# Performance work log

Hardware: AMD Instinct MI355X
Metric: run time of the kernel (lower is better)

Reference implementation:

```python
import jax, jax.numpy as jnp
import numpy as np

N_NODES = 20000
N_EDGES = 320000
IN_DIM = 512
HID = 256
N_GRAPHS = 256


def setup_inputs() -> dict:
    key = jax.random.key(0)
    ks = jax.random.split(key, 7)
    x = jax.random.normal(ks[0], (N_NODES, IN_DIM), dtype=jnp.float32)
    edge_index = jax.random.randint(ks[1], (2, N_EDGES), 0, N_NODES, dtype=jnp.int64)
    batch = jnp.sort(jax.random.randint(ks[2], (N_NODES,), 0, N_GRAPHS, dtype=jnp.int64))
    W = jax.random.normal(ks[3], (IN_DIM, HID), dtype=jnp.float32) * (1.0 / np.sqrt(IN_DIM))
    b = jax.random.normal(ks[4], (HID,), dtype=jnp.float32) * 0.02
    lin_w = jax.random.normal(ks[5], (HID, 1), dtype=jnp.float32) * (1.0 / np.sqrt(HID))
    lin_b = jax.random.normal(ks[6], (1,), dtype=jnp.float32) * 0.02
    return {"x": x, "edge_index": edge_index, "batch": batch,
            "W": W, "b": b, "lin_w": lin_w, "lin_b": lin_b}


def reference(x, edge_index, batch, W, b, lin_w, lin_b):
    N = x.shape[0]
    # --- GCNConv: add self-loops, symmetric normalization ---
    loop = jnp.arange(N, dtype=edge_index.dtype)
    src = jnp.concatenate([edge_index[0], loop])   # [E+N]
    dst = jnp.concatenate([edge_index[1], loop])   # [E+N]
    deg = jax.ops.segment_sum(jnp.ones_like(dst, dtype=x.dtype), dst, num_segments=N)
    dinv = jnp.where(deg > 0, jax.lax.rsqrt(deg), 0.0)          # [N]
    norm = dinv[src] * dinv[dst]                                 # [E+N]
    h = x @ W                                                    # [N, HID] dense GEMM
    msgs = h[src] * norm[:, None]                                # gather + scale
    agg = jax.ops.segment_sum(msgs, dst, num_segments=N) + b     # scatter-add
    xr = jax.nn.relu(agg)                                        # [N, HID]
    # --- global_mean_pool over graph ids ---
    sums = jax.ops.segment_sum(xr, batch, num_segments=N_GRAPHS)             # [G, HID]
    counts = jax.ops.segment_sum(jnp.ones((N,), dtype=x.dtype), batch, num_segments=N_GRAPHS)
    pooled = sums / jnp.maximum(counts, 1.0)[:, None]
    # --- linear head + sigmoid ---
    out = jax.nn.sigmoid(pooled @ lin_w + lin_b)                 # [G, 1]
    return out.reshape(-1)
```

## Files before the change

kernel.cpp:

```cpp
#include <hip/hip_runtime.h>
#include <hip/hip_bf16.h>
#include <cstdint>

typedef __attribute__((ext_vector_type(8))) _Float16 half8;
typedef __attribute__((ext_vector_type(2))) float f32x2;
typedef __attribute__((ext_vector_type(4))) float f32x4;

#define N_NODES 20000
#define N_EDGES 320000
#define IN_DIM 512
#define HID 256
#define N_GRAPHS 256
#define NPB 8
#define ECH 1024
#define BSTR 40

#define PREP_W   (IN_DIM * HID)
#define PREP_E   (PREP_W + N_EDGES)
#define PREP_B   (PREP_E + N_NODES)
__global__ __launch_bounds__(256) void prep_kernel(const float* __restrict__ W,
                                                   const int* __restrict__ dst,
                                                   const int* __restrict__ batch,
                                                   _Float16* __restrict__ wt,
                                                   int* __restrict__ ecnt,
                                                   int* __restrict__ counts) {
    int t = blockIdx.x * 256 + threadIdx.x;
    if (t < PREP_W) {
        wt[t] = (_Float16)W[(t & 511) * HID + (t >> 9)];
    } else if (t < PREP_E) {
        atomicAdd(&ecnt[dst[t - PREP_W]], 1);
    } else if (t < PREP_B) {
        atomicAdd(&counts[batch[t - PREP_E]], 1);
    }
}

__global__ __launch_bounds__(1024) void scan_dinv_kernel(const int* __restrict__ ecnt,
                                                         int* __restrict__ offsets,
                                                         float* __restrict__ dinv) {
    __shared__ int wsum[16];
    int t = threadIdx.x;
    int lane = t & 63, wid = t >> 6;
    const int CHS = 20;
    int base = t * CHS;
    int vals[CHS];
    int s = 0;
    if (t < 1000) {
        const int4* p = reinterpret_cast<const int4*>(ecnt + base);
#pragma unroll
        for (int i = 0; i < 5; ++i) {
            int4 v = p[i];
            vals[4*i+0] = v.x; vals[4*i+1] = v.y; vals[4*i+2] = v.z; vals[4*i+3] = v.w;
        }
#pragma unroll
        for (int i = 0; i < CHS; ++i) s += vals[i];
    }
    int incl = s;
#pragma unroll
    for (int off = 1; off < 64; off <<= 1) {
        int u = __shfl_up(incl, off, 64);
        if (lane >= off) incl += u;
    }
    if (lane == 63) wsum[wid] = incl;
    __syncthreads();
    if (t < 16) {
        int v = wsum[t];
#pragma unroll
        for (int off = 1; off < 16; off <<= 1) {
            int u = __shfl_up(v, off, 16);
            if (t >= off) v += u;
        }
        wsum[t] = v;
    }
    __syncthreads();
    int woff = (wid == 0) ? 0 : wsum[wid - 1];
    if (t < 1000) {
        int run = woff + incl - s;
#pragma unroll
        for (int i = 0; i < CHS; ++i) {
            int idx = base + i;
            offsets[idx] = run;
            dinv[idx] = rsqrtf((float)(vals[i] + 1));
            run += vals[i];
        }
    }
    if (t == 1023) offsets[N_NODES] = wsum[15];
}

#define GEMM_BLOCKS ((N_NODES + 63) / 64)
#define CSR_BLOCKS  ((N_EDGES + 255) / 256)
__global__ __launch_bounds__(256) void gemm_csr_kernel(const float* __restrict__ x,
                                                       const _Float16* __restrict__ wt,
                                                       unsigned char* __restrict__ h8,
                                                       const int* __restrict__ src,
                                                       const int* __restrict__ dst,
                                                       const float* __restrict__ dinv,
                                                       const int* __restrict__ offsets,
                                                       int* __restrict__ cnt2,
                                                       int2* __restrict__ csr) {
    __shared__ _Float16 bsl[256 * BSTR];
    if (blockIdx.x >= GEMM_BLOCKS) {
        int e = (blockIdx.x - GEMM_BLOCKS) * 256 + threadIdx.x;
        if (e < N_EDGES) {
            int s = src[e], d = dst[e];
            int slot = offsets[d] + atomicAdd(&cnt2[d], 1);
            int2 pk;
            pk.x = s;
            pk.y = __float_as_int(dinv[s] * dinv[d]);
            csr[slot] = pk;
        }
        return;
    }
    const int K = IN_DIM;
    int t    = threadIdx.x;
    int wave = t >> 6;
    int lane = t & 63;
    int col  = lane & 15;
    int quad = lane >> 4;
    int row0 = blockIdx.x * 64 + wave * 16;

    f32x4 acc[16];
#pragma unroll
    for (int i = 0; i < 16; ++i) acc[i] = (f32x4){0.f, 0.f, 0.f, 0.f};

    int arow = row0 + col;
    if (arow >= N_NODES) arow = N_NODES - 1;
    const float* aptr = x + (size_t)arow * K + quad * 8;
    const uint4* wsrc = reinterpret_cast<const uint4*>(wt + (size_t)t * K);

    float4 pa0 = *reinterpret_cast<const float4*>(aptr);
    float4 pa1 = *reinterpret_cast<const float4*>(aptr + 4);
    uint4 b0 = wsrc[0], b1 = wsrc[1], b2 = wsrc[2], b3 = wsrc[3];

    for (int k0 = 0; k0 < K; k0 += 32) {
        __syncthreads();
        {
            uint4* d = reinterpret_cast<uint4*>(&bsl[t * BSTR]);
            d[0] = b0; d[1] = b1; d[2] = b2; d[3] = b3;
        }
        __syncthreads();
        half8 xf;
        xf[0] = (_Float16)pa0.x; xf[1] = (_Float16)pa0.y;
        xf[2] = (_Float16)pa0.z; xf[3] = (_Float16)pa0.w;
        xf[4] = (_Float16)pa1.x; xf[5] = (_Float16)pa1.y;
        xf[6] = (_Float16)pa1.z; xf[7] = (_Float16)pa1.w;
        if (k0 + 32 < K) {
            const float* ap = aptr + k0 + 32;
            pa0 = *reinterpret_cast<const float4*>(ap);
            pa1 = *reinterpret_cast<const float4*>(ap + 4);
            const uint4* ws = wsrc + ((k0 + 32) >> 3);
            b0 = ws[0]; b1 = ws[1]; b2 = ws[2]; b3 = ws[3];
        }
#pragma unroll
        for (int nt = 0; nt < 16; ++nt) {
            half8 wf = *reinterpret_cast<const half8*>(
                &bsl[(nt * 16 + col) * BSTR + quad * 8]);
            acc[nt] = __builtin_amdgcn_mfma_f32_16x16x32_f16(wf, xf, acc[nt], 0, 0, 0);
        }
    }

    int node = row0 + col;
    if (node < N_NODES) {
        int fb = quad * 4;
        unsigned char* hrow = h8 + (size_t)node * HID + fb;
#pragma unroll
        for (int nt = 0; nt < 16; ++nt) {
            int u = __builtin_amdgcn_cvt_pk_fp8_f32(acc[nt][0], acc[nt][1], 0, false);
            u = __builtin_amdgcn_cvt_pk_fp8_f32(acc[nt][2], acc[nt][3], u, true);
            *reinterpret_cast<unsigned int*>(hrow + nt * 16) = (unsigned int)u;
        }
    }
}

__global__ __launch_bounds__(256, 8) void aggregate_kernel(const unsigned char* __restrict__ h8,
                                                           const float* __restrict__ bias,
                                                           const float* __restrict__ dinv,
                                                           const int* __restrict__ offsets,
                                                           const int2* __restrict__ csr,
                                                           const int* __restrict__ batch,
                                                           float* __restrict__ sums) {
    __shared__ int2 s_e[ECH];
    float* pool = reinterpret_cast<float*>(s_e);
    int v0  = blockIdx.x * NPB;
    int t   = threadIdx.x;
    int grp = t >> 6;
    int fl  = t & 63;
    int vg  = v0 + grp * 2;
    const float4 bf = *reinterpret_cast<const float4*>(bias + 4 * fl);

    int off[3];
#pragma unroll
    for (int i = 0; i <= 2; ++i) off[i] = offsets[vg + i];
    int beg0 = offsets[v0], end0 = offsets[v0 + NPB];

    float a0[2], a1[2], a2[2], a3[2];
#pragma unroll
    for (int i = 0; i < 2; ++i) {
        int v = vg + i;
        float dv = dinv[v];
        float d2 = dv * dv;
        unsigned int u = *reinterpret_cast<const unsigned int*>(h8 + (size_t)v * HID + 4 * fl);
        f32x2 lo = __builtin_amdgcn_cvt_pk_f32_fp8(u, false);
        f32x2 hi = __builtin_amdgcn_cvt_pk_f32_fp8(u, true);
        a0[i] = d2 * lo[0]; a1[i] = d2 * lo[1];
        a2[i] = d2 * hi[0]; a3[i] = d2 * hi[1];
    }

    for (int cb = beg0; cb < end0; cb += ECH) {
        int n = min(ECH, end0 - cb);
        for (int tt = t; tt < n; tt += 256) s_e[tt] = csr[cb + tt];
        __syncthreads();
#pragma unroll
        for (int i = 0; i < 2; ++i) {
            int lo_ = off[i] - cb;     if (lo_ < 0) lo_ = 0;
            int hi_ = off[i + 1] - cb; if (hi_ > n) hi_ = n;
            float x0 = a0[i], x1 = a1[i], x2 = a2[i], x3 = a3[i];
            int j = lo_;
            for (; j + 8 <= hi_; j += 8) {
#pragma unroll
                for (int q = 0; q < 8; ++q) {
                    int2 e = s_e[j + q];
                    unsigned int u = *reinterpret_cast<const unsigned int*>(
                        h8 + (size_t)e.x * HID + 4 * fl);
                    float w = __int_as_float(e.y);
                    f32x2 lo = __builtin_amdgcn_cvt_pk_f32_fp8(u, false);
                    f32x2 hi = __builtin_amdgcn_cvt_pk_f32_fp8(u, true);
                    x0 += w * lo[0]; x1 += w * lo[1];
                    x2 += w * hi[0]; x3 += w * hi[1];
                }
            }
            for (; j < hi_; ++j) {
                int2 e = s_e[j];
                unsigned int u = *reinterpret_cast<const unsigned int*>(
                    h8 + (size_t)e.x * HID + 4 * fl);
                float w = __int_as_float(e.y);
                f32x2 lo = __builtin_amdgcn_cvt_pk_f32_fp8(u, false);
                f32x2 hi = __builtin_amdgcn_cvt_pk_f32_fp8(u, true);
                x0 += w * lo[0]; x1 += w * lo[1];
                x2 += w * hi[0]; x3 += w * hi[1];
            }
            a0[i] = x0; a1[i] = x1; a2[i] = x2; a3[i] = x3;
        }
        __syncthreads();
    }

#pragma unroll
    for (int i = 0; i < 2; ++i) {
        f32x4 r;
        r[0] = fmaxf(a0[i] + bf.x, 0.f);
        r[1] = fmaxf(a1[i] + bf.y, 0.f);
        r[2] = fmaxf(a2[i] + bf.z, 0.f);
        r[3] = fmaxf(a3[i] + bf.w, 0.f);
        *reinterpret_cast<f32x4*>(&pool[(grp * 2 + i) * HID + 4 * fl]) = r;
    }
    __syncthreads();

    float acc = 0.f;
    int cur_g = batch[v0];
#pragma unroll
    for (int i = 0; i < NPB; ++i) {
        float val = pool[i * HID + t];
        int g = batch[v0 + i];
        if (g != cur_g) {
            atomicAdd(&sums[(size_t)cur_g * HID + t], acc);
            acc = 0.f;
            cur_g = g;
        }
        acc += val;
    }
    atomicAdd(&sums[(size_t)cur_g * HID + t], acc);
}

__global__ __launch_bounds__(256) void head_kernel(const float* __restrict__ sums,
                                                   const int* __restrict__ counts,
                                                   const float* __restrict__ lin_w,
                                                   const float* __restrict__ lin_b,
                                                   float* __restrict__ out) {
    int g = blockIdx.x;
    int f = threadIdx.x;
    float c = (float)counts[g];
    if (c < 1.f) c = 1.f;
    float v = (sums[(size_t)g * HID + f] / c) * lin_w[f];
#pragma unroll
    for (int off = 32; off >= 1; off >>= 1) v += __shfl_down(v, off, 64);
    __shared__ float red[4];
    if ((f & 63) == 0) red[f >> 6] = v;
    __syncthreads();
    if (f == 0) {
        float s = red[0] + red[1] + red[2] + red[3] + lin_b[0];
        out[g] = 1.0f / (1.0f + expf(-s));
    }
}

extern "C" void kernel_launch(void* const* d_in, const int* in_sizes, int n_in,
                              void* d_out, int out_size, void* d_ws, size_t ws_size,
                              hipStream_t stream) {
    const float* x     = (const float*)d_in[0];
    const int*   edge  = (const int*)d_in[1];
    const int*   batch = (const int*)d_in[2];
    const float* W     = (const float*)d_in[3];
    const float* b     = (const float*)d_in[4];
    const float* lin_w = (const float*)d_in[5];
    const float* lin_b = (const float*)d_in[6];
    float*       out   = (float*)d_out;

    const int N = N_NODES, E = N_EDGES, G = N_GRAPHS, K = IN_DIM, H = HID;
    const int* src = edge;
    const int* dst = edge + E;

    char* p = (char*)d_ws;
    auto alloc = [&](size_t bytes) {
        char* r = p;
        p += (bytes + 255) & ~(size_t)255;
        return r;
    };
    _Float16*      wt      = (_Float16*)alloc((size_t)H * K * 2);
    unsigned char* h8      = (unsigned char*)alloc((size_t)N * H);
    float*         dinv    = (float*)alloc((size_t)N * 4);
    int*           offsets = (int*)alloc((size_t)(N + 1) * 4);
    int2*          csr     = (int2*)alloc((size_t)E * 8);
    char* z0 = p;
    int*   ecnt   = (int*)alloc((size_t)N * 4);
    int*   cnt2   = (int*)alloc((size_t)N * 4);
    float* sums   = (float*)alloc((size_t)G * H * 4);
    int*   counts = (int*)alloc((size_t)G * 4);
    size_t zbytes = (size_t)(p - z0);

    hipMemsetAsync(z0, 0, zbytes, stream);

    prep_kernel<<<(PREP_B + 255) / 256, 256, 0, stream>>>(W, dst, batch, wt, ecnt, counts);
    scan_dinv_kernel<<<1, 1024, 0, stream>>>(ecnt, offsets, dinv);
    gemm_csr_kernel<<<GEMM_BLOCKS + CSR_BLOCKS, 256, 0, stream>>>(x, wt, h8, src, dst,
                                                                  dinv, offsets, cnt2, csr);
    aggregate_kernel<<<N / NPB, 256, 0, stream>>>(h8, b, dinv, offsets, csr, batch, sums);
    head_kernel<<<G, 256, 0, stream>>>(sums, counts, lin_w, lin_b, out);
}
```

Measured before the change: 186.2 us.

## Split GEMM and CSR fill into separate kernels with 16-row GEMM tiles

Separates the fused GEMM/CSR-fill launch into two kernels. The GEMM tile shrinks from 64 rows to 16 rows per block, with each wave covering a quarter of the output columns, so there are four times as many blocks and only 4 accumulators per thread. The W transpose in prep now reads coalesced and writes scattered. The aim is better occupancy and load balance for the GEMM, at the cost of loading the full W tile into shared memory for every 16 rows and paying one extra launch.

```diff
diff --git a/kernel.cpp b/kernel.cpp
--- a/kernel.cpp
+++ b/kernel.cpp
@@ -26,7 +26,8 @@
                                                    int* __restrict__ counts) {
     int t = blockIdx.x * 256 + threadIdx.x;
     if (t < PREP_W) {
-        wt[t] = (_Float16)W[(t & 511) * HID + (t >> 9)];
+        int k = t >> 8, n = t & 255;
+        wt[n * IN_DIM + k] = (_Float16)W[t];
     } else if (t < PREP_E) {
         atomicAdd(&ecnt[dst[t - PREP_W]], 1);
     } else if (t < PREP_B) {
@@ -86,44 +87,41 @@
     if (t == 1023) offsets[N_NODES] = wsum[15];
 }
 
-#define GEMM_BLOCKS ((N_NODES + 63) / 64)
-#define CSR_BLOCKS  ((N_EDGES + 255) / 256)
-__global__ __launch_bounds__(256) void gemm_csr_kernel(const float* __restrict__ x,
-                                                       const _Float16* __restrict__ wt,
-                                                       unsigned char* __restrict__ h8,
-                                                       const int* __restrict__ src,
+__global__ __launch_bounds__(256) void csr_fill_kernel(const int* __restrict__ src,
                                                        const int* __restrict__ dst,
                                                        const float* __restrict__ dinv,
                                                        const int* __restrict__ offsets,
                                                        int* __restrict__ cnt2,
                                                        int2* __restrict__ csr) {
+    int e = blockIdx.x * 256 + threadIdx.x;
+    if (e < N_EDGES) {
+        int s = src[e], d = dst[e];
+        int slot = offsets[d] + atomicAdd(&cnt2[d], 1);
+        int2 pk;
+        pk.x = s;
+        pk.y = __float_as_int(dinv[s] * dinv[d]);
+        csr[slot] = pk;
+    }
+}
+
+#define GEMM_BLOCKS (N_NODES / 16)
+__global__ __launch_bounds__(256) void gemm_kernel(const float* __restrict__ x,
+                                                   const _Float16* __restrict__ wt,
+                                                   unsigned char* __restrict__ h8) {
     __shared__ _Float16 bsl[256 * BSTR];
-    if (blockIdx.x >= GEMM_BLOCKS) {
-        int e = (blockIdx.x - GEMM_BLOCKS) * 256 + threadIdx.x;
-        if (e < N_EDGES) {
-            int s = src[e], d = dst[e];
-            int slot = offsets[d] + atomicAdd(&cnt2[d], 1);
-            int2 pk;
-            pk.x = s;
-            pk.y = __float_as_int(dinv[s] * dinv[d]);
-            csr[slot] = pk;
-        }
-        return;
-    }
     const int K = IN_DIM;
     int t    = threadIdx.x;
     int wave = t >> 6;
     int lane = t & 63;
     int col  = lane & 15;
     int quad = lane >> 4;
-    int row0 = blockIdx.x * 64 + wave * 16;
-
-    f32x4 acc[16];
-#pragma unroll
-    for (int i = 0; i < 16; ++i) acc[i] = (f32x4){0.f, 0.f, 0.f, 0.f};
+    int row0 = blockIdx.x * 16;
+
+    f32x4 acc[4];
+#pragma unroll
+    for (int i = 0; i < 4; ++i) acc[i] = (f32x4){0.f, 0.f, 0.f, 0.f};
 
     int arow = row0 + col;
-    if (arow >= N_NODES) arow = N_NODES - 1;
     const float* aptr = x + (size_t)arow * K + quad * 8;
     const uint4* wsrc = reinterpret_cast<const uint4*>(wt + (size_t)t * K);
 
@@ -151,23 +149,21 @@
             b0 = ws[0]; b1 = ws[1]; b2 = ws[2]; b3 = ws[3];
         }
 #pragma unroll
-        for (int nt = 0; nt < 16; ++nt) {
+        for (int i = 0; i < 4; ++i) {
+            int nt = wave * 4 + i;
             half8 wf = *reinterpret_cast<const half8*>(
                 &bsl[(nt * 16 + col) * BSTR + quad * 8]);
-            acc[nt] = __builtin_amdgcn_mfma_f32_16x16x32_f16(wf, xf, acc[nt], 0, 0, 0);
+            acc[i] = __builtin_amdgcn_mfma_f32_16x16x32_f16(wf, xf, acc[i], 0, 0, 0);
         }
     }
 
     int node = row0 + col;
-    if (node < N_NODES) {
-        int fb = quad * 4;
-        unsigned char* hrow = h8 + (size_t)node * HID + fb;
-#pragma unroll
-        for (int nt = 0; nt < 16; ++nt) {
-            int u = __builtin_amdgcn_cvt_pk_fp8_f32(acc[nt][0], acc[nt][1], 0, false);
-            u = __builtin_amdgcn_cvt_pk_fp8_f32(acc[nt][2], acc[nt][3], u, true);
-            *reinterpret_cast<unsigned int*>(hrow + nt * 16) = (unsigned int)u;
-        }
+    unsigned char* hrow = h8 + (size_t)node * HID + wave * 64 + quad * 4;
+#pragma unroll
+    for (int i = 0; i < 4; ++i) {
+        int u = __builtin_amdgcn_cvt_pk_fp8_f32(acc[i][0], acc[i][1], 0, false);
+        u = __builtin_amdgcn_cvt_pk_fp8_f32(acc[i][2], acc[i][3], u, true);
+        *reinterpret_cast<unsigned int*>(hrow + i * 16) = (unsigned int)u;
     }
 }
 
@@ -329,8 +325,8 @@
 
     prep_kernel<<<(PREP_B + 255) / 256, 256, 0, stream>>>(W, dst, batch, wt, ecnt, counts);
     scan_dinv_kernel<<<1, 1024, 0, stream>>>(ecnt, offsets, dinv);
-    gemm_csr_kernel<<<GEMM_BLOCKS + CSR_BLOCKS, 256, 0, stream>>>(x, wt, h8, src, dst,
-                                                                  dinv, offsets, cnt2, csr);
+    csr_fill_kernel<<<(E + 255) / 256, 256, 0, stream>>>(src, dst, dinv, offsets, cnt2, csr);
+    gemm_kernel<<<GEMM_BLOCKS, 256, 0, stream>>>(x, wt, h8);
     aggregate_kernel<<<N / NPB, 256, 0, stream>>>(h8, b, dinv, offsets, csr, batch, sums);
     head_kernel<<<G, 256, 0, stream>>>(sums, counts, lin_w, lin_b, out);
 }
```

Result: slower. 229.9 us (+23.5%).

## Retile GEMM so each wave covers 80 rows by 64 columns

Applied to the files above, without the earlier changes.

The GEMM tile changes from 64 rows per block, with each wave computing 16 rows across all 256 columns, to 80 rows per block, with each wave computing all 80 rows across its own 64-column slice. Every wave now reuses each B fragment from LDS across 5 row tiles instead of reading 16 fragments per k-step, which cuts LDS traffic per MFMA and gives fewer blocks. In exchange, every wave loads the full 80-row A tile from global memory, so A reads per block are duplicated four times (mostly served by cache), and register pressure rises. The bounds clamp is dropped because 20000 divides evenly by 80.

```diff
diff --git a/kernel.cpp b/kernel.cpp
--- a/kernel.cpp
+++ b/kernel.cpp
@@ -86,7 +86,7 @@
     if (t == 1023) offsets[N_NODES] = wsum[15];
 }
 
-#define GEMM_BLOCKS ((N_NODES + 63) / 64)
+#define GEMM_BLOCKS (N_NODES / 80)
 #define CSR_BLOCKS  ((N_EDGES + 255) / 256)
 __global__ __launch_bounds__(256) void gemm_csr_kernel(const float* __restrict__ x,
                                                        const _Float16* __restrict__ wt,
@@ -116,19 +116,24 @@
     int lane = t & 63;
     int col  = lane & 15;
     int quad = lane >> 4;
-    int row0 = blockIdx.x * 64 + wave * 16;
-
-    f32x4 acc[16];
-#pragma unroll
-    for (int i = 0; i < 16; ++i) acc[i] = (f32x4){0.f, 0.f, 0.f, 0.f};
-
-    int arow = row0 + col;
-    if (arow >= N_NODES) arow = N_NODES - 1;
-    const float* aptr = x + (size_t)arow * K + quad * 8;
+    int row0 = blockIdx.x * 80;
+
+    f32x4 acc[5][4];
+#pragma unroll
+    for (int j = 0; j < 5; ++j)
+#pragma unroll
+        for (int i = 0; i < 4; ++i) acc[j][i] = (f32x4){0.f, 0.f, 0.f, 0.f};
+
+    const float* aptr = x + (size_t)(row0 + col) * K + quad * 8;
     const uint4* wsrc = reinterpret_cast<const uint4*>(wt + (size_t)t * K);
 
-    float4 pa0 = *reinterpret_cast<const float4*>(aptr);
-    float4 pa1 = *reinterpret_cast<const float4*>(aptr + 4);
+    float4 pa0[5], pa1[5];
+#pragma unroll
+    for (int j = 0; j < 5; ++j) {
+        const float* ap = aptr + (size_t)j * 16 * K;
+        pa0[j] = *reinterpret_cast<const float4*>(ap);
+        pa1[j] = *reinterpret_cast<const float4*>(ap + 4);
+    }
     uint4 b0 = wsrc[0], b1 = wsrc[1], b2 = wsrc[2], b3 = wsrc[3];
 
     for (int k0 = 0; k0 < K; k0 += 32) {
@@ -138,35 +143,44 @@
             d[0] = b0; d[1] = b1; d[2] = b2; d[3] = b3;
         }
         __syncthreads();
-        half8 xf;
-        xf[0] = (_Float16)pa0.x; xf[1] = (_Float16)pa0.y;
-        xf[2] = (_Float16)pa0.z; xf[3] = (_Float16)pa0.w;
-        xf[4] = (_Float16)pa1.x; xf[5] = (_Float16)pa1.y;
-        xf[6] = (_Float16)pa1.z; xf[7] = (_Float16)pa1.w;
+        half8 xf[5];
+#pragma unroll
+        for (int j = 0; j < 5; ++j) {
+            xf[j][0] = (_Float16)pa0[j].x; xf[j][1] = (_Float16)pa0[j].y;
+            xf[j][2] = (_Float16)pa0[j].z; xf[j][3] = (_Float16)pa0[j].w;
+            xf[j][4] = (_Float16)pa1[j].x; xf[j][5] = (_Float16)pa1[j].y;
+            xf[j][6] = (_Float16)pa1[j].z; xf[j][7] = (_Float16)pa1[j].w;
+        }
         if (k0 + 32 < K) {
-            const float* ap = aptr + k0 + 32;
-            pa0 = *reinterpret_cast<const float4*>(ap);
-            pa1 = *reinterpret_cast<const float4*>(ap + 4);
+#pragma unroll
+            for (int j = 0; j < 5; ++j) {
+                const float* ap = aptr + (size_t)j * 16 * K + k0 + 32;
+                pa0[j] = *reinterpret_cast<const float4*>(ap);
+                pa1[j] = *reinterpret_cast<const float4*>(ap + 4);
+            }
             const uint4* ws = wsrc + ((k0 + 32) >> 3);
             b0 = ws[0]; b1 = ws[1]; b2 = ws[2]; b3 = ws[3];
         }
 #pragma unroll
-        for (int nt = 0; nt < 16; ++nt) {
+        for (int i = 0; i < 4; ++i) {
             half8 wf = *reinterpret_cast<const half8*>(
-                &bsl[(nt * 16 + col) * BSTR + quad * 8]);
-            acc[nt] = __builtin_amdgcn_mfma_f32_16x16x32_f16(wf, xf, acc[nt], 0, 0, 0);
-        }
-    }
-
-    int node = row0 + col;
-    if (node < N_NODES) {
-        int fb = quad * 4;
-        unsigned char* hrow = h8 + (size_t)node * HID + fb;
-#pragma unroll
-        for (int nt = 0; nt < 16; ++nt) {
-            int u = __builtin_amdgcn_cvt_pk_fp8_f32(acc[nt][0], acc[nt][1], 0, false);
-            u = __builtin_amdgcn_cvt_pk_fp8_f32(acc[nt][2], acc[nt][3], u, true);
-            *reinterpret_cast<unsigned int*>(hrow + nt * 16) = (unsigned int)u;
+                &bsl[((wave * 4 + i) * 16 + col) * BSTR + quad * 8]);
+#pragma unroll
+            for (int j = 0; j < 5; ++j)
+                acc[j][i] = __builtin_amdgcn_mfma_f32_16x16x32_f16(wf, xf[j],
+                                                                   acc[j][i], 0, 0, 0);
+        }
+    }
+
+#pragma unroll
+    for (int j = 0; j < 5; ++j) {
+        int node = row0 + j * 16 + col;
+        unsigned char* hrow = h8 + (size_t)node * HID + wave * 64 + quad * 4;
+#pragma unroll
+        for (int i = 0; i < 4; ++i) {
+            int u = __builtin_amdgcn_cvt_pk_fp8_f32(acc[j][i][0], acc[j][i][1], 0, false);
+            u = __builtin_amdgcn_cvt_pk_fp8_f32(acc[j][i][2], acc[j][i][3], u, true);
+            *reinterpret_cast<unsigned int*>(hrow + i * 16) = (unsigned int)u;
         }
     }
 }
```

Result: slower. 203.9 us (+9.5%).
